# Optimization experiments

Hardware: AMD Instinct MI355X
Metric: run time of the kernel (lower is better)

The kernel has to match this reference:

```python
import jax, jax.numpy as jnp
import numpy as np

HIDDEN_DIM = 512  # H; hidden/encoder feature dim is 2H = 1024


def setup_inputs() -> dict:
    key = jax.random.key(0)
    k1, k2, k3, k4, k5 = jax.random.split(key, 5)
    B, S, D2, H = 16, 4096, 2 * HIDDEN_DIM, HIDDEN_DIM
    hidden = jax.random.normal(k1, (B, D2), dtype=jnp.float32)
    encoder_outputs = jax.random.normal(k2, (B, S, D2), dtype=jnp.float32)
    # nn.Linear(4H, H): weight [H, 4H] in torch; store transposed [4H, H] for x @ W
    W_attn = jax.random.normal(k3, (2 * D2, H), dtype=jnp.float32) * (1.0 / np.sqrt(2 * D2))
    b_attn = jax.random.normal(k4, (H,), dtype=jnp.float32) * 0.01
    # nn.Linear(H, 1, bias=False): weight [1, H] -> vector [H]
    w_v = jax.random.normal(k5, (H,), dtype=jnp.float32) * (1.0 / np.sqrt(H))
    return {"hidden": hidden, "encoder_outputs": encoder_outputs,
            "W_attn": W_attn, "b_attn": b_attn, "w_v": w_v}


def reference(hidden, encoder_outputs, W_attn, b_attn, w_v):
    B, S, D2 = encoder_outputs.shape
    # Broadcast decoder hidden over seq positions and concat with encoder outputs.
    hid = jnp.broadcast_to(hidden[:, None, :], (B, S, D2))
    cat = jnp.concatenate([hid, encoder_outputs], axis=2)        # [B, S, 4H]
    energy = jnp.tanh(cat @ W_attn + b_attn)                      # [B, S, H]
    scores = jnp.einsum('bsh,h->bs', energy, w_v)                 # [B, S]
    attention = jax.nn.softmax(scores, axis=1)                    # [B, S]
    context = jnp.einsum('bs,bsd->bd', attention, encoder_outputs)  # [B, 2H]
    return context
```

## Files before the change

kernel.cpp:

```cpp
#include <hip/hip_runtime.h>
#include <hip/hip_bf16.h>
#include <math.h>

#define HD   512
#define D2   1024
#define SEQ  4096
#define BAT  16
#define BM   128
#define BK   32
#define NKT  32

typedef _Float16 half8 __attribute__((ext_vector_type(8)));
typedef float    f32x4 __attribute__((ext_vector_type(4)));
typedef __attribute__((address_space(3))) void lds_void_t;
typedef __attribute__((address_space(1))) void glb_void_t;

__global__ void wconv_kernel(const float* __restrict__ W, _Float16* __restrict__ WtS) {
  __shared__ float tile[32][17];
  const int kt  = blockIdx.x;
  const int nbg = blockIdx.y;
  const int nh  = nbg >> 4, nbl = nbg & 15;
  const int t   = threadIdx.x;
  {
    const int n16 = t & 15, kk = t >> 4;
    #pragma unroll
    for (int i = 0; i < 2; ++i) {
      const int k = kk + i * 16;
      tile[k][n16] = W[(size_t)(D2 + kt * 32 + k) * HD + nh * 256 + nbl * 16 + n16];
    }
  }
  __syncthreads();
  if (t < 64) {
    const int kc = t >> 4, nlo = t & 15;
    half8 h;
    #pragma unroll
    for (int j = 0; j < 8; ++j) h[j] = (_Float16)tile[kc * 8 + j][nlo];
    *(half8*)(WtS + ((size_t)(kt * 2 + nh) * 1024 + nbl * 64 + kc * 16 + nlo) * 8) = h;
  }
}

__global__ void hproj_kernel(const float* __restrict__ hidden,
                             const float* __restrict__ W,
                             float* __restrict__ hproj) {
  const int b  = blockIdx.x >> 3;
  const int kc = blockIdx.x & 7;
  const int h  = threadIdx.x;
  float a0 = 0.f, a1 = 0.f;
  #pragma unroll 4
  for (int i = 0; i < 128; ++i) {
    const int d = kc * 128 + i;
    const float hd = hidden[b * D2 + d];
    a0 += hd * W[(size_t)d * HD + h];
    a1 += hd * W[(size_t)d * HD + h + 256];
  }
  atomicAdd(&hproj[b * HD + h], a0);
  atomicAdd(&hproj[b * HD + h + 256], a1);
}

__global__ __launch_bounds__(512, 2) void scores_kernel(
    const float* __restrict__ enc, const _Float16* __restrict__ WtS,
    const float* __restrict__ hproj, const float* __restrict__ b_attn,
    const float* __restrict__ w_v, float* __restrict__ scores)
{
  __shared__ __align__(16) float    As[3][BM * BK];
  __shared__ __align__(16) _Float16 Bs[3][2048 * 8];

  const int s0  = blockIdx.x * BM;
  const int b   = blockIdx.y;
  const int tid = threadIdx.x, lane = tid & 63, w = tid >> 6;
  const int col16 = lane & 15, q = lane >> 4;
  const int wm = w >> 2, wn = w & 3;

  const float* encB = enc + ((size_t)b * SEQ + s0) * D2;

  f32x4 acc[4][8];
  const f32x4 z = {0.f, 0.f, 0.f, 0.f};
  #pragma unroll
  for (int mi = 0; mi < 4; ++mi)
    #pragma unroll
    for (int ni = 0; ni < 8; ++ni) acc[mi][ni] = z;

  auto stage = [&](int kt, int buf) {
    const float* ek = encB + kt * BK;
    #pragma unroll
    for (int i = 0; i < 2; ++i) {
      const int s = i * 512 + tid;
      const int row = s >> 3;
      const int g = (s & 7) ^ (row & 7);
      __builtin_amdgcn_global_load_lds((glb_void_t*)(ek + (size_t)row * D2 + g * 4),
          (lds_void_t*)((char*)&As[buf][0] + s * 16), 16, 0, 0);
    }
    const _Float16* wk = WtS + (size_t)kt * 16384;
    #pragma unroll
    for (int i = 0; i < 4; ++i) {
      const int c = i * 512 + tid;
      __builtin_amdgcn_global_load_lds((glb_void_t*)(wk + c * 8),
          (lds_void_t*)((char*)&Bs[buf][0] + c * 16), 16, 0, 0);
    }
  };

  auto compute = [&](int buf) {
    const float* pA = &As[buf][0];
    const _Float16* pB = &Bs[buf][0];
    half8 af[4];
    #pragma unroll
    for (int mi = 0; mi < 4; ++mi) {
      const int row = wm * 64 + mi * 16 + col16;
      const int rb = row * 8, rx = row & 7;
      const f32x4 lo = *(const f32x4*)&pA[(rb + ((2 * q)     ^ rx)) * 4];
      const f32x4 hi = *(const f32x4*)&pA[(rb + ((2 * q + 1) ^ rx)) * 4];
      half8 h;
      h[0] = (_Float16)lo[0]; h[1] = (_Float16)lo[1];
      h[2] = (_Float16)lo[2]; h[3] = (_Float16)lo[3];
      h[4] = (_Float16)hi[0]; h[5] = (_Float16)hi[1];
      h[6] = (_Float16)hi[2]; h[7] = (_Float16)hi[3];
      af[mi] = h;
    }
    #pragma unroll
    for (int ni = 0; ni < 8; ++ni) {
      const half8 bf = *(const half8*)&pB[((wn * 8 + ni) * 64 + q * 16 + col16) * 8];
      #pragma unroll
      for (int mi = 0; mi < 4; ++mi)
        acc[mi][ni] = __builtin_amdgcn_mfma_f32_16x16x32_f16(af[mi], bf, acc[mi][ni], 0, 0, 0);
    }
  };

  stage(0, 0);
  stage(1, 1);
  asm volatile("s_waitcnt vmcnt(6)" ::: "memory");
  __builtin_amdgcn_s_barrier();

  #pragma unroll 3
  for (int kt = 0; kt < NKT - 2; ++kt) {
    stage(kt + 2, (kt + 2) % 3);
    compute(kt % 3);
    asm volatile("s_waitcnt vmcnt(6)" ::: "memory");
    __builtin_amdgcn_s_barrier();
  }
  compute((NKT - 2) % 3);
  asm volatile("s_waitcnt vmcnt(0)" ::: "memory");
  __builtin_amdgcn_s_barrier();
  compute((NKT - 1) % 3);

  float p[4][4];
  #pragma unroll
  for (int mi = 0; mi < 4; ++mi)
    #pragma unroll
    for (int r = 0; r < 4; ++r) p[mi][r] = 0.f;

  #pragma unroll
  for (int ni = 0; ni < 8; ++ni) {
    const int n = wn * 128 + ni * 16 + col16;
    const float hb = hproj[b * HD + n] + b_attn[n];
    const float wv = w_v[n];
    #pragma unroll
    for (int mi = 0; mi < 4; ++mi) {
      #pragma unroll
      for (int r = 0; r < 4; ++r) {
        float x = fminf(fmaxf(acc[mi][ni][r] + hb, -15.f), 15.f);
        float ex = __expf(2.f * x);
        p[mi][r] += wv * __fdividef(ex - 1.f, ex + 1.f);
      }
    }
  }
  #pragma unroll
  for (int off = 8; off >= 1; off >>= 1) {
    #pragma unroll
    for (int mi = 0; mi < 4; ++mi)
      #pragma unroll
      for (int r = 0; r < 4; ++r)
        p[mi][r] += __shfl_xor(p[mi][r], off, 64);
  }
  if (col16 == 0) {
    const int m0 = s0 + wm * 64 + q * 4;
    #pragma unroll
    for (int mi = 0; mi < 4; ++mi)
      #pragma unroll
      for (int r = 0; r < 4; ++r)
        atomicAdd(&scores[b * SEQ + m0 + mi * 16 + r], p[mi][r]);
  }
}

__global__ void softmax_kernel(float* __restrict__ scores) {
  const int b = blockIdx.x;
  float* sc = scores + b * SEQ;
  __shared__ float red[16];
  const int tid = threadIdx.x;
  float loc[16];
  float mx = -1e30f;
  #pragma unroll
  for (int i = 0; i < 16; ++i) { loc[i] = sc[i * 256 + tid]; mx = fmaxf(mx, loc[i]); }
  #pragma unroll
  for (int off = 32; off >= 1; off >>= 1) mx = fmaxf(mx, __shfl_xor(mx, off, 64));
  if ((tid & 63) == 0) red[tid >> 6] = mx;
  __syncthreads();
  mx = fmaxf(fmaxf(red[0], red[1]), fmaxf(red[2], red[3]));
  float sum = 0.f;
  #pragma unroll
  for (int i = 0; i < 16; ++i) { loc[i] = __expf(loc[i] - mx); sum += loc[i]; }
  #pragma unroll
  for (int off = 32; off >= 1; off >>= 1) sum += __shfl_xor(sum, off, 64);
  if ((tid & 63) == 0) red[8 + (tid >> 6)] = sum;
  __syncthreads();
  sum = red[8] + red[9] + red[10] + red[11];
  const float inv = 1.0f / sum;
  #pragma unroll
  for (int i = 0; i < 16; ++i) sc[i * 256 + tid] = loc[i] * inv;
}

__global__ __launch_bounds__(256) void context_kernel(const float* __restrict__ attn,
                                                      const float* __restrict__ enc,
                                                      float* __restrict__ out) {
  const int b  = blockIdx.y;
  const int s0 = blockIdx.x * 64;
  const int tid = threadIdx.x;
  const float* encB = enc + ((size_t)b * SEQ + s0) * D2 + tid * 4;
  const float* at   = attn + b * SEQ + s0;
  f32x4 acc0 = {0.f, 0.f, 0.f, 0.f}, acc1 = {0.f, 0.f, 0.f, 0.f};
  #pragma unroll 8
  for (int i = 0; i < 64; i += 2) {
    acc0 += at[i]     * *(const f32x4*)(encB + (size_t)i * D2);
    acc1 += at[i + 1] * *(const f32x4*)(encB + (size_t)(i + 1) * D2);
  }
  f32x4 acc = acc0 + acc1;
  float* o = out + b * D2 + tid * 4;
  atomicAdd(o + 0, acc[0]);
  atomicAdd(o + 1, acc[1]);
  atomicAdd(o + 2, acc[2]);
  atomicAdd(o + 3, acc[3]);
}

extern "C" void kernel_launch(void* const* d_in, const int* in_sizes, int n_in,
                              void* d_out, int out_size, void* d_ws, size_t ws_size,
                              hipStream_t stream) {
  (void)in_sizes; (void)n_in; (void)ws_size;
  const float* hidden = (const float*)d_in[0];
  const float* enc    = (const float*)d_in[1];
  const float* W      = (const float*)d_in[2];
  const float* b_attn = (const float*)d_in[3];
  const float* w_v    = (const float*)d_in[4];
  float* out = (float*)d_out;

  char* ws = (char*)d_ws;
  _Float16* WtS = (_Float16*)ws;
  float* hproj  = (float*)(ws + (1 << 20));
  float* scores = (float*)(ws + (1 << 20) + 32768);

  hipMemsetAsync(d_out, 0, (size_t)out_size * sizeof(float), stream);
  hipMemsetAsync(hproj, 0, BAT * HD * sizeof(float), stream);
  hipMemsetAsync(scores, 0, (size_t)BAT * SEQ * sizeof(float), stream);

  wconv_kernel  <<<dim3(32, 32),          256, 0, stream>>>(W, WtS);
  hproj_kernel  <<<dim3(128),             256, 0, stream>>>(hidden, W, hproj);
  scores_kernel <<<dim3(SEQ / BM, BAT),   512, 0, stream>>>(enc, WtS, hproj, b_attn, w_v, scores);
  softmax_kernel<<<dim3(BAT),             256, 0, stream>>>(scores);
  context_kernel<<<dim3(SEQ / 64, BAT),   256, 0, stream>>>(scores, enc, out);
}
```

Baseline: 486.1 us.

## Interleave split A/B staging with half-tile MFMA and LDS score reduction

Restructures the scores GEMM main loop to split global-to-LDS staging of A and B, read B fragments in two halves, and prefetch the next A fragments while MFMAs run. Barriers and s_setprio raise MFMA priority so memory issue overlaps with compute. The epilogue replaces per-row global atomics with an LDS reduction across the four N-warps and a plain store, which also removes the scores memset. The cost is more barriers per k-tile and higher register pressure from double-buffered A fragments.

Result: no change. 489.2 us (+0.6%).

```diff
diff --git a/kernel.cpp b/kernel.cpp
--- a/kernel.cpp
+++ b/kernel.cpp
@@ -80,7 +80,7 @@
     #pragma unroll
     for (int ni = 0; ni < 8; ++ni) acc[mi][ni] = z;
 
-  auto stage = [&](int kt, int buf) {
+  auto stageA = [&](int kt, int buf) {
     const float* ek = encB + kt * BK;
     #pragma unroll
     for (int i = 0; i < 2; ++i) {
@@ -90,6 +90,8 @@
       __builtin_amdgcn_global_load_lds((glb_void_t*)(ek + (size_t)row * D2 + g * 4),
           (lds_void_t*)((char*)&As[buf][0] + s * 16), 16, 0, 0);
     }
+  };
+  auto stageB = [&](int kt, int buf) {
     const _Float16* wk = WtS + (size_t)kt * 16384;
     #pragma unroll
     for (int i = 0; i < 4; ++i) {
@@ -98,11 +100,8 @@
           (lds_void_t*)((char*)&Bs[buf][0] + c * 16), 16, 0, 0);
     }
   };
-
-  auto compute = [&](int buf) {
+  auto readA = [&](int buf, half8* af) {
     const float* pA = &As[buf][0];
-    const _Float16* pB = &Bs[buf][0];
-    half8 af[4];
     #pragma unroll
     for (int mi = 0; mi < 4; ++mi) {
       const int row = wm * 64 + mi * 16 + col16;
@@ -116,31 +115,80 @@
       h[6] = (_Float16)hi[2]; h[7] = (_Float16)hi[3];
       af[mi] = h;
     }
-    #pragma unroll
-    for (int ni = 0; ni < 8; ++ni) {
-      const half8 bf = *(const half8*)&pB[((wn * 8 + ni) * 64 + q * 16 + col16) * 8];
+  };
+  auto readB = [&](int buf, int half_, half8* bf) {
+    const _Float16* pB = &Bs[buf][0];
+    #pragma unroll
+    for (int ni = 0; ni < 4; ++ni)
+      bf[ni] = *(const half8*)&pB[((wn * 8 + half_ * 4 + ni) * 64 + q * 16 + col16) * 8];
+  };
+  auto mfma16 = [&](const half8* af, const half8* bf, int nbase) {
+    #pragma unroll
+    for (int ni = 0; ni < 4; ++ni)
       #pragma unroll
       for (int mi = 0; mi < 4; ++mi)
-        acc[mi][ni] = __builtin_amdgcn_mfma_f32_16x16x32_f16(af[mi], bf, acc[mi][ni], 0, 0, 0);
-    }
-  };
-
-  stage(0, 0);
-  stage(1, 1);
+        acc[mi][nbase + ni] =
+            __builtin_amdgcn_mfma_f32_16x16x32_f16(af[mi], bf[ni], acc[mi][nbase + ni], 0, 0, 0);
+  };
+
+  half8 afA[4], afB[4];
+  half8 bl[4], bh[4];
+
+  stageA(0, 0); stageB(0, 0);
+  stageA(1, 1); stageB(1, 1);
   asm volatile("s_waitcnt vmcnt(6)" ::: "memory");
   __builtin_amdgcn_s_barrier();
-
-  #pragma unroll 3
-  for (int kt = 0; kt < NKT - 2; ++kt) {
-    stage(kt + 2, (kt + 2) % 3);
-    compute(kt % 3);
-    asm volatile("s_waitcnt vmcnt(6)" ::: "memory");
-    __builtin_amdgcn_s_barrier();
-  }
-  compute((NKT - 2) % 3);
+  readA(0, afA);
+
+  for (int jo = 0; jo < 5; ++jo) {
+    #pragma unroll
+    for (int u = 0; u < 6; ++u) {
+      const int kt = jo * 6 + u;
+      const int bc = u % 3;
+      const int bn = (u + 1) % 3;
+      const int bs = (u + 2) % 3;
+      half8* afC = (u & 1) ? afB : afA;
+      half8* afN = (u & 1) ? afA : afB;
+      readB(bc, 0, bl);
+      readB(bc, 1, bh);
+      stageA(kt + 2, bs);
+      __builtin_amdgcn_s_barrier();
+      __builtin_amdgcn_s_setprio(1);
+      mfma16(afC, bl, 0);
+      __builtin_amdgcn_s_setprio(0);
+      __builtin_amdgcn_s_barrier();
+      stageB(kt + 2, bs);
+      asm volatile("s_waitcnt vmcnt(6)" ::: "memory");
+      __builtin_amdgcn_s_barrier();
+      __builtin_amdgcn_s_setprio(1);
+      mfma16(afC, bh, 4);
+      readA(bn, afN);
+      __builtin_amdgcn_s_setprio(0);
+      __builtin_amdgcn_s_barrier();
+    }
+  }
+
+  readB(0, 0, bl);
+  readB(0, 1, bh);
+  __builtin_amdgcn_s_barrier();
+  __builtin_amdgcn_s_setprio(1);
+  mfma16(afA, bl, 0);
+  __builtin_amdgcn_s_setprio(0);
+  __builtin_amdgcn_s_barrier();
   asm volatile("s_waitcnt vmcnt(0)" ::: "memory");
   __builtin_amdgcn_s_barrier();
-  compute((NKT - 1) % 3);
+  __builtin_amdgcn_s_setprio(1);
+  mfma16(afA, bh, 4);
+  readA(1, afB);
+  __builtin_amdgcn_s_setprio(0);
+  __builtin_amdgcn_s_barrier();
+  readB(1, 0, bl);
+  readB(1, 1, bh);
+  __builtin_amdgcn_s_barrier();
+  __builtin_amdgcn_s_setprio(1);
+  mfma16(afB, bl, 0);
+  mfma16(afB, bh, 4);
+  __builtin_amdgcn_s_setprio(0);
 
   float p[4][4];
   #pragma unroll
@@ -171,13 +219,20 @@
       for (int r = 0; r < 4; ++r)
         p[mi][r] += __shfl_xor(p[mi][r], off, 64);
   }
+
+  float* red = (float*)&As[0][0];
+  __syncthreads();
   if (col16 == 0) {
-    const int m0 = s0 + wm * 64 + q * 4;
     #pragma unroll
     for (int mi = 0; mi < 4; ++mi)
       #pragma unroll
       for (int r = 0; r < 4; ++r)
-        atomicAdd(&scores[b * SEQ + m0 + mi * 16 + r], p[mi][r]);
+        red[wn * 128 + wm * 64 + mi * 16 + q * 4 + r] = p[mi][r];
+  }
+  __syncthreads();
+  if (tid < 128) {
+    const float v = red[tid] + red[128 + tid] + red[256 + tid] + red[384 + tid];
+    scores[b * SEQ + s0 + tid] = v;
   }
 }
 
@@ -248,7 +303,6 @@
 
   hipMemsetAsync(d_out, 0, (size_t)out_size * sizeof(float), stream);
   hipMemsetAsync(hproj, 0, BAT * HD * sizeof(float), stream);
-  hipMemsetAsync(scores, 0, (size_t)BAT * SEQ * sizeof(float), stream);
 
   wconv_kernel  <<<dim3(32, 32),          256, 0, stream>>>(W, WtS);
   hproj_kernel  <<<dim3(128),             256, 0, stream>>>(hidden, W, hproj);
```

## Load B fragments directly to registers, deepen A pipeline, reduce scores without atomics

Applied to the files above, without the earlier changes.

The scores GEMM no longer stages the fp16 weight tile in LDS. Each wave loads its B fragments straight into double-buffered registers, while the A tile gets a 4-deep LDS ring. K iteration starts at a per-block rotated offset so blocks fetch different weight slices at once, and MFMA sections are wrapped in s_setprio. The per-row score reduction across the four N-waves now goes through LDS with a plain store, which removes the atomics and the scores memset, at the cost of more VGPR pressure under launch_bounds(512,2).

New measurement: 470.0 us. 1.03x faster.

```diff
diff --git a/kernel.cpp b/kernel.cpp
--- a/kernel.cpp
+++ b/kernel.cpp
@@ -62,11 +62,11 @@
     const float* __restrict__ hproj, const float* __restrict__ b_attn,
     const float* __restrict__ w_v, float* __restrict__ scores)
 {
-  __shared__ __align__(16) float    As[3][BM * BK];
-  __shared__ __align__(16) _Float16 Bs[3][2048 * 8];
+  __shared__ __align__(16) float As[4][BM * BK];
 
   const int s0  = blockIdx.x * BM;
   const int b   = blockIdx.y;
+  const int kt0 = (blockIdx.x + blockIdx.y) & 31;
   const int tid = threadIdx.x, lane = tid & 63, w = tid >> 6;
   const int col16 = lane & 15, q = lane >> 4;
   const int wm = w >> 2, wn = w & 3;
@@ -80,28 +80,25 @@
     #pragma unroll
     for (int ni = 0; ni < 8; ++ni) acc[mi][ni] = z;
 
-  auto stage = [&](int kt, int buf) {
-    const float* ek = encB + kt * BK;
+  auto stageA = [&](int ktp, int buf) {
+    const float* ek = encB + ktp * BK;
     #pragma unroll
     for (int i = 0; i < 2; ++i) {
       const int s = i * 512 + tid;
       const int row = s >> 3;
       const int g = (s & 7) ^ (row & 7);
       __builtin_amdgcn_global_load_lds((glb_void_t*)(ek + (size_t)row * D2 + g * 4),
-          (lds_void_t*)((char*)&As[buf][0] + s * 16), 16, 0, 0);
-    }
-    const _Float16* wk = WtS + (size_t)kt * 16384;
-    #pragma unroll
-    for (int i = 0; i < 4; ++i) {
-      const int c = i * 512 + tid;
-      __builtin_amdgcn_global_load_lds((glb_void_t*)(wk + c * 8),
-          (lds_void_t*)((char*)&Bs[buf][0] + c * 16), 16, 0, 0);
+          (lds_void_t*)((char*)&As[0][0] + (size_t)buf * 16384 + s * 16), 16, 0, 0);
     }
   };
-
-  auto compute = [&](int buf) {
-    const float* pA = &As[buf][0];
-    const _Float16* pB = &Bs[buf][0];
+  auto loadB = [&](int ktp, half8* bf) {
+    const _Float16* wk = WtS + (size_t)ktp * 16384;
+    #pragma unroll
+    for (int ni = 0; ni < 8; ++ni)
+      bf[ni] = *(const half8*)(wk + ((size_t)((wn * 8 + ni) * 64 + q * 16 + col16)) * 8);
+  };
+  auto compute = [&](int buf, const half8* bf) {
+    const float* pA = &As[0][0] + (size_t)buf * 4096;
     half8 af[4];
     #pragma unroll
     for (int mi = 0; mi < 4; ++mi) {
@@ -116,31 +113,55 @@
       h[6] = (_Float16)hi[2]; h[7] = (_Float16)hi[3];
       af[mi] = h;
     }
-    #pragma unroll
-    for (int ni = 0; ni < 8; ++ni) {
-      const half8 bf = *(const half8*)&pB[((wn * 8 + ni) * 64 + q * 16 + col16) * 8];
+    __builtin_amdgcn_s_setprio(1);
+    #pragma unroll
+    for (int ni = 0; ni < 8; ++ni)
       #pragma unroll
       for (int mi = 0; mi < 4; ++mi)
-        acc[mi][ni] = __builtin_amdgcn_mfma_f32_16x16x32_f16(af[mi], bf, acc[mi][ni], 0, 0, 0);
-    }
+        acc[mi][ni] = __builtin_amdgcn_mfma_f32_16x16x32_f16(af[mi], bf[ni], acc[mi][ni], 0, 0, 0);
+    __builtin_amdgcn_s_setprio(0);
   };
 
-  stage(0, 0);
-  stage(1, 1);
-  asm volatile("s_waitcnt vmcnt(6)" ::: "memory");
-  __builtin_amdgcn_s_barrier();
-
-  #pragma unroll 3
-  for (int kt = 0; kt < NKT - 2; ++kt) {
-    stage(kt + 2, (kt + 2) % 3);
-    compute(kt % 3);
-    asm volatile("s_waitcnt vmcnt(6)" ::: "memory");
+  half8 BE[8], BO[8];
+
+  stageA(kt0, 0);
+  stageA((kt0 + 1) & 31, 1);
+  stageA((kt0 + 2) & 31, 2);
+  loadB(kt0, BE);
+
+  for (int kt = 0; kt < 28; kt += 2) {
+    loadB((kt + 1 + kt0) & 31, BO);
     __builtin_amdgcn_s_barrier();
-  }
-  compute((NKT - 2) % 3);
+    stageA((kt + 3 + kt0) & 31, (kt + 3) & 3);
+    asm volatile("s_waitcnt vmcnt(12)" ::: "memory");
+    compute(kt & 3, BE);
+
+    loadB((kt + 2 + kt0) & 31, BE);
+    __builtin_amdgcn_s_barrier();
+    stageA((kt + 4 + kt0) & 31, (kt + 4) & 3);
+    asm volatile("s_waitcnt vmcnt(12)" ::: "memory");
+    compute((kt + 1) & 3, BO);
+  }
+
+  loadB((29 + kt0) & 31, BO);
+  __builtin_amdgcn_s_barrier();
+  stageA((31 + kt0) & 31, 3);
+  asm volatile("s_waitcnt vmcnt(12)" ::: "memory");
+  compute(0, BE);
+
+  loadB((30 + kt0) & 31, BE);
+  __builtin_amdgcn_s_barrier();
+  asm volatile("s_waitcnt vmcnt(10)" ::: "memory");
+  compute(1, BO);
+
+  loadB((31 + kt0) & 31, BO);
+  __builtin_amdgcn_s_barrier();
+  asm volatile("s_waitcnt vmcnt(8)" ::: "memory");
+  compute(2, BE);
+
+  __builtin_amdgcn_s_barrier();
   asm volatile("s_waitcnt vmcnt(0)" ::: "memory");
-  __builtin_amdgcn_s_barrier();
-  compute((NKT - 1) % 3);
+  compute(3, BO);
 
   float p[4][4];
   #pragma unroll
@@ -171,13 +192,20 @@
       for (int r = 0; r < 4; ++r)
         p[mi][r] += __shfl_xor(p[mi][r], off, 64);
   }
+
+  float* red = (float*)&As[0][0];
+  __syncthreads();
   if (col16 == 0) {
-    const int m0 = s0 + wm * 64 + q * 4;
     #pragma unroll
     for (int mi = 0; mi < 4; ++mi)
       #pragma unroll
       for (int r = 0; r < 4; ++r)
-        atomicAdd(&scores[b * SEQ + m0 + mi * 16 + r], p[mi][r]);
+        red[wn * 128 + wm * 64 + mi * 16 + q * 4 + r] = p[mi][r];
+  }
+  __syncthreads();
+  if (tid < 128) {
+    const float v = red[tid] + red[128 + tid] + red[256 + tid] + red[384 + tid];
+    scores[b * SEQ + s0 + tid] = v;
   }
 }
 
@@ -248,7 +276,6 @@
 
   hipMemsetAsync(d_out, 0, (size_t)out_size * sizeof(float), stream);
   hipMemsetAsync(hproj, 0, BAT * HD * sizeof(float), stream);
-  hipMemsetAsync(scores, 0, (size_t)BAT * SEQ * sizeof(float), stream);
 
   wconv_kernel  <<<dim3(32, 32),          256, 0, stream>>>(W, WtS);
   hproj_kernel  <<<dim3(128),             256, 0, stream>>>(hidden, W, hproj);
```
